# Performance work log

Hardware: AMD Instinct MI355X
Metric: run time of the kernel (lower is better)

## Reference

```python
import jax, jax.numpy as jnp
import numpy as np

INPUT_SIZE = 256
HIDDEN = 256


def setup_inputs() -> dict:
    key = jax.random.key(0)
    ks = jax.random.split(key, 9)
    B, T = 32, 2048
    d_in = INPUT_SIZE + HIDDEN
    s = 1.0 / np.sqrt(d_in)  # nn.Linear default init scale
    def W(k):
        return jax.random.uniform(k, (d_in, HIDDEN), jnp.float32, -s, s)
    def b(k):
        return jax.random.uniform(k, (HIDDEN,), jnp.float32, -s, s)
    return {
        "x": jax.random.normal(ks[0], (B, T, INPUT_SIZE), jnp.float32),
        "W_f": W(ks[1]), "b_f": b(ks[2]),
        "W_i": W(ks[3]), "b_i": b(ks[4]),
        "W_o": W(ks[5]), "b_o": b(ks[6]),
        "W_c": W(ks[7]), "b_c": b(ks[8]),
    }


def reference(x, W_f, b_f, W_i, b_i, W_o, b_o, W_c, b_c):
    B, T, _ = x.shape
    H = W_f.shape[1]
    # Fuse the 4 gate GEMMs into one [d_in, 4H] matmul (same math).
    W4 = jnp.concatenate([W_f, W_i, W_o, W_c], axis=1)  # [in+H, 4H]
    b4 = jnp.concatenate([b_f, b_i, b_o, b_c], axis=0)  # [4H]

    def step(carry, x_t):
        c, h = carry
        z = jnp.concatenate([x_t, h], axis=1) @ W4 + b4  # [B, 4H]
        f = jax.nn.sigmoid(z[:, 0 * H:1 * H])
        i = jax.nn.sigmoid(z[:, 1 * H:2 * H])
        o = jax.nn.sigmoid(z[:, 2 * H:3 * H])
        g = jnp.tanh(z[:, 3 * H:4 * H])
        c = f * c + i * g
        h = o * jnp.tanh(c)
        return (c, h), h

    c0 = jnp.zeros((B, H), x.dtype)
    h0 = jnp.zeros((B, H), x.dtype)
    _, hs = jax.lax.scan(step, (c0, h0), jnp.swapaxes(x, 0, 1))  # [T, B, H]
    # Original prepends each new hidden state, so output is in REVERSE time order.
    out = jnp.swapaxes(hs, 0, 1)[:, ::-1, :]  # [B, T, H]
    return out
```

## Files before the change

kernel.cpp:

```cpp
#include <hip/hip_runtime.h>
#include <cstdint>
#include <cstddef>

#define NB    32
#define NTT   2048
#define NIN   256
#define NH    256
#define NG    16
#define BLOCK 512
#define NHC   16

typedef __attribute__((ext_vector_type(8))) short    s8v;
typedef __attribute__((ext_vector_type(4))) float    f4v;
typedef __attribute__((ext_vector_type(4))) unsigned u4v;

__device__ __forceinline__ float u2f(unsigned u) {
    union { float f; unsigned u; } x; x.u = u; return x.f;
}
__device__ __forceinline__ unsigned cvt_pk_bf16(float s0, float s1) {
    unsigned r;
    asm("v_cvt_pk_bf16_f32 %0, %1, %2" : "=v"(r) : "v"(s0), "v"(s1));
    return r;
}
__device__ __forceinline__ void split2(float v0, float v1, unsigned& hp, unsigned& lp) {
    hp = cvt_pk_bf16(v0, v1);
    float h0 = u2f(hp << 16);
    float h1 = u2f(hp & 0xFFFF0000u);
    lp = cvt_pk_bf16(v0 - h0, v1 - h1);
}
__device__ __forceinline__ void split8(f4v a, f4v b, u4v& hw, u4v& lw) {
    unsigned h0,h1,h2,h3,l0,l1,l2,l3;
    split2(a[0], a[1], h0, l0);
    split2(a[2], a[3], h1, l1);
    split2(b[0], b[1], h2, l2);
    split2(b[2], b[3], h3, l3);
    hw = (u4v){h0,h1,h2,h3};
    lw = (u4v){l0,l1,l2,l3};
}
__device__ __forceinline__ float fast_sig(float v) {
    const float L2E = 1.4426950408889634f;
    return __builtin_amdgcn_rcpf(1.f + __builtin_amdgcn_exp2f(-L2E * v));
}
__device__ __forceinline__ float fast_tanh(float v) {
    const float L2E2 = 2.8853900817779268f;
    float e = __builtin_amdgcn_exp2f(L2E2 * v);
    return 1.f - 2.f * __builtin_amdgcn_rcpf(e + 1.f);
}

__device__ __forceinline__ u4v ld4_dev(const unsigned* p) {
    u4v v;
    asm volatile("global_load_dwordx4 %0, %1, off sc1" : "=v"(v) : "v"(p));
    return v;
}
__device__ __forceinline__ int ldf_dev(const int* p) {
    int v;
    asm volatile("global_load_dword %0, %1, off sc1\n\ts_waitcnt vmcnt(0)"
                 : "=v"(v) : "v"(p) : "memory");
    return v;
}
__device__ __forceinline__ void st_dev(unsigned* p, unsigned v) {
    asm volatile("global_store_dword %0, %1, off sc1" :: "v"(p), "v"(v) : "memory");
}
template<int OFF>
__device__ __forceinline__ void pf_ld4x2(const float* base, f4v& a, f4v& b) {
    asm volatile(
        "global_load_dwordx4 %0, %2, off offset:%c3\n\t"
        "global_load_dwordx4 %1, %2, off offset:%c4"
        : "=&v"(a), "=&v"(b)
        : "v"(base), "n"(OFF), "n"(OFF+16)
        : "memory");
}


__global__ __launch_bounds__(BLOCK, 1) void lstm_kernel(
    const float* __restrict__ x,
    const float* __restrict__ Wf, const float* __restrict__ bfp,
    const float* __restrict__ Wi, const float* __restrict__ bip,
    const float* __restrict__ Wo, const float* __restrict__ bop,
    const float* __restrict__ Wc, const float* __restrict__ bcp,
    float* __restrict__ out,
    unsigned* __restrict__ wsbase)
{
    __shared__ unsigned short Ahi[NB * 512];
    __shared__ unsigned short Alo[NB * 512];
    __shared__ float zbuf[32][68];

    char* AhiB = (char*)Ahi;
    char* AloB = (char*)Alo;
    const int wg   = blockIdx.x;
    const int tid  = threadIdx.x;
    const int lane = tid & 63;
    const int wv   = tid >> 6;
    const int mt   = wv & 1;
    const int nt   = wv >> 1;

    int* flags     = (int*)wsbase;
    unsigned* hbuf = wsbase + 1024;

    s8v bhi[16], blo[16];
    for (int p = 0; p < 2; ++p) {
        {
            const int lc   = tid >> 4;
            const int gate = 2 * p + (lc >> 4);
            const int col  = wg * NHC + (lc & 15);
            const float* W = (gate == 0) ? Wf : (gate == 1) ? Wi : (gate == 2) ? Wo : Wc;
            #pragma unroll
            for (int cj = 0; cj < 4; ++cj) {
                const int kc = (tid & 15) * 4 + cj;
                const int k0 = kc * 8;
                f4v a, b;
                #pragma unroll
                for (int e = 0; e < 4; ++e) a[e] = W[(size_t)(k0 + e) * NH + col];
                #pragma unroll
                for (int e = 0; e < 4; ++e) b[e] = W[(size_t)(k0 + 4 + e) * NH + col];
                u4v hwv, lwv;
                split8(a, b, hwv, lwv);
                *(u4v*)(AhiB + lc * 1024 + ((kc ^ (lc & 7)) << 4)) = hwv;
                *(u4v*)(AloB + lc * 1024 + ((kc ^ (lc & 7)) << 4)) = lwv;
            }
        }
        __syncthreads();
        if ((nt >> 1) == p) {
            const int brow = (nt & 1) * 16 + (lane & 15);
            const int bsub = lane >> 4;
            #pragma unroll
            for (int kt = 0; kt < 16; ++kt) {
                const int kc = kt * 4 + bsub;
                bhi[kt] = *(s8v*)(AhiB + brow * 1024 + ((kc ^ (brow & 7)) << 4));
                blo[kt] = *(s8v*)(AloB + brow * 1024 + ((kc ^ (brow & 7)) << 4));
            }
        }
        __syncthreads();
    }

    const int ub   = tid >> 4;
    const int ulh  = tid & 15;
    const int ucol = wg * NHC + ulh;
    const float bias_f = bfp[ucol];
    const float bias_i = bip[ucol];
    const float bias_o = bop[ucol];
    const float bias_c = bcp[ucol];
    float cst = 0.f;

    const int sb   = tid >> 4;
    const int sseg = tid & 15;

    const int arow = mt * 16 + (lane & 15);
    const int asub = lane >> 4;

    f4v xv[4];
    {
        const float* xr = x + (size_t)sb * NTT * NIN + sseg * 16;
        xv[0] = *(const f4v*)(xr);
        xv[1] = *(const f4v*)(xr + 4);
        xv[2] = *(const f4v*)(xr + 8);
        xv[3] = *(const f4v*)(xr + 12);
    }

    for (int t = 0; t < NTT; ++t) {
        #pragma unroll
        for (int j = 0; j < 2; ++j) {
            u4v hwv, lwv;
            split8(xv[2 * j], xv[2 * j + 1], hwv, lwv);
            const int kc = sseg * 2 + j;
            *(u4v*)(AhiB + sb * 1024 + ((kc ^ (sb & 7)) << 4)) = hwv;
            *(u4v*)(AloB + sb * 1024 + ((kc ^ (sb & 7)) << 4)) = lwv;
        }
        {
            const int tp = (t < NTT - 1) ? t + 1 : t;
            const float* xr = x + ((size_t)sb * NTT + tp) * NIN + sseg * 16;
            pf_ld4x2<0>(xr, xv[0], xv[1]);
            pf_ld4x2<32>(xr, xv[2], xv[3]);
        }
        __syncthreads();

        if (t > 0 && wv == 0 && lane < NG) {
            const int* fp = flags + lane;
            int it = 0;
            for (;;) {
                int v = ldf_dev(fp);
                if (!__any(v < t)) break;
                if (++it > 4096) break;
            }
        }
        __syncthreads();

        f4v acc0 = (f4v){0.f, 0.f, 0.f, 0.f};
        f4v acc1 = acc0, acc2 = acc0;

        if (t > 0) {
            const unsigned* hp = hbuf + (size_t)(t & 1) * (NB * NH)
                               + (size_t)sb * NH + sseg * 16;
            u4v w0 = ld4_dev(hp);
            u4v w1 = ld4_dev(hp + 4);
            u4v w2 = ld4_dev(hp + 8);
            u4v w3 = ld4_dev(hp + 12);

            #pragma unroll
            for (int kt = 0; kt < 8; ++kt) {
                const int kc = kt * 4 + asub;
                s8v ah = *(s8v*)(AhiB + arow * 1024 + ((kc ^ (arow & 7)) << 4));
                s8v al = *(s8v*)(AloB + arow * 1024 + ((kc ^ (arow & 7)) << 4));
                acc0 = __builtin_amdgcn_mfma_f32_16x16x32_bf16(ah, bhi[kt], acc0, 0, 0, 0);
                acc1 = __builtin_amdgcn_mfma_f32_16x16x32_bf16(ah, blo[kt], acc1, 0, 0, 0);
                acc2 = __builtin_amdgcn_mfma_f32_16x16x32_bf16(al, bhi[kt], acc2, 0, 0, 0);
            }

            asm volatile("s_waitcnt vmcnt(0)"
                         : "+v"(w0), "+v"(w1), "+v"(w2), "+v"(w3) :: "memory");
            u4v wA[2][2] = {{w0, w1}, {w2, w3}};
            #pragma unroll
            for (int j = 0; j < 2; ++j) {
                u4v hwv, lwv;
                hwv[0] = __builtin_amdgcn_perm(wA[j][0][1], wA[j][0][0], 0x05040100u);
                hwv[1] = __builtin_amdgcn_perm(wA[j][0][3], wA[j][0][2], 0x05040100u);
                hwv[2] = __builtin_amdgcn_perm(wA[j][1][1], wA[j][1][0], 0x05040100u);
                hwv[3] = __builtin_amdgcn_perm(wA[j][1][3], wA[j][1][2], 0x05040100u);
                lwv[0] = __builtin_amdgcn_perm(wA[j][0][1], wA[j][0][0], 0x07060302u);
                lwv[1] = __builtin_amdgcn_perm(wA[j][0][3], wA[j][0][2], 0x07060302u);
                lwv[2] = __builtin_amdgcn_perm(wA[j][1][1], wA[j][1][0], 0x07060302u);
                lwv[3] = __builtin_amdgcn_perm(wA[j][1][3], wA[j][1][2], 0x07060302u);
                const int kc = 32 + sseg * 2 + j;
                *(u4v*)(AhiB + sb * 1024 + ((kc ^ (sb & 7)) << 4)) = hwv;
                *(u4v*)(AloB + sb * 1024 + ((kc ^ (sb & 7)) << 4)) = lwv;
            }
        } else {
            #pragma unroll
            for (int kt = 0; kt < 8; ++kt) {
                const int kc = kt * 4 + asub;
                s8v ah = *(s8v*)(AhiB + arow * 1024 + ((kc ^ (arow & 7)) << 4));
                s8v al = *(s8v*)(AloB + arow * 1024 + ((kc ^ (arow & 7)) << 4));
                acc0 = __builtin_amdgcn_mfma_f32_16x16x32_bf16(ah, bhi[kt], acc0, 0, 0, 0);
                acc1 = __builtin_amdgcn_mfma_f32_16x16x32_bf16(ah, blo[kt], acc1, 0, 0, 0);
                acc2 = __builtin_amdgcn_mfma_f32_16x16x32_bf16(al, bhi[kt], acc2, 0, 0, 0);
            }
            const u4v zz = (u4v){0u, 0u, 0u, 0u};
            #pragma unroll
            for (int j = 0; j < 2; ++j) {
                const int kc = 32 + sseg * 2 + j;
                *(u4v*)(AhiB + sb * 1024 + ((kc ^ (sb & 7)) << 4)) = zz;
                *(u4v*)(AloB + sb * 1024 + ((kc ^ (sb & 7)) << 4)) = zz;
            }
        }
        __syncthreads();

        #pragma unroll
        for (int kt = 8; kt < 16; ++kt) {
            const int kc = kt * 4 + asub;
            s8v ah = *(s8v*)(AhiB + arow * 1024 + ((kc ^ (arow & 7)) << 4));
            s8v al = *(s8v*)(AloB + arow * 1024 + ((kc ^ (arow & 7)) << 4));
            acc0 = __builtin_amdgcn_mfma_f32_16x16x32_bf16(ah, bhi[kt], acc0, 0, 0, 0);
            acc1 = __builtin_amdgcn_mfma_f32_16x16x32_bf16(ah, blo[kt], acc1, 0, 0, 0);
            acc2 = __builtin_amdgcn_mfma_f32_16x16x32_bf16(al, bhi[kt], acc2, 0, 0, 0);
        }
        const f4v zv = acc0 + acc1 + acc2;

        {
            const int zc = nt * 16 + (lane & 15);
            const int rb = mt * 16 + (lane >> 4) * 4;
            #pragma unroll
            for (int j = 0; j < 4; ++j)
                zbuf[rb + j][zc] = zv[j];
        }
        __syncthreads();

        {
            const float zf = zbuf[ub][ulh]      + bias_f;
            const float zi = zbuf[ub][16 + ulh] + bias_i;
            const float zo = zbuf[ub][32 + ulh] + bias_o;
            const float zg = zbuf[ub][48 + ulh] + bias_c;
            const float fg = fast_sig(zf);
            const float ig = fast_sig(zi);
            const float og = fast_sig(zo);
            const float gg = fast_tanh(zg);
            cst = fg * cst + ig * gg;
            const float hv = og * fast_tanh(cst);
            out[((size_t)ub * NTT + (NTT - 1 - t)) * NH + ucol] = hv;
            unsigned p0  = cvt_pk_bf16(hv, 0.f);
            float   hif  = u2f(p0 << 16);
            unsigned w   = cvt_pk_bf16(hv, hv - hif);
            st_dev(hbuf + (size_t)((t + 1) & 1) * (NB * NH) + (size_t)ub * NH + ucol, w);
        }
        asm volatile("s_waitcnt vmcnt(0)"
                     : "+v"(xv[0]), "+v"(xv[1]), "+v"(xv[2]), "+v"(xv[3]) :: "memory");
        __syncthreads();
        if (tid == 0)
            st_dev((unsigned*)(flags + wg), (unsigned)(t + 1));
    }
}

extern "C" void kernel_launch(void* const* d_in, const int* in_sizes, int n_in,
                              void* d_out, int out_size, void* d_ws, size_t ws_size,
                              hipStream_t stream) {
    (void)in_sizes; (void)n_in; (void)out_size; (void)ws_size;
    const float* x  = (const float*)d_in[0];
    const float* Wf = (const float*)d_in[1];
    const float* bf = (const float*)d_in[2];
    const float* Wi = (const float*)d_in[3];
    const float* bi = (const float*)d_in[4];
    const float* Wo = (const float*)d_in[5];
    const float* bo = (const float*)d_in[6];
    const float* Wc = (const float*)d_in[7];
    const float* bc = (const float*)d_in[8];
    float* out = (float*)d_out;
    unsigned* ws = (unsigned*)d_ws;

    hipMemsetAsync(d_ws, 0, 4096, stream);

    lstm_kernel<<<NG, BLOCK, 0, stream>>>(x, Wf, bf, Wi, bi, Wo, bo, Wc, bc,
                                          out, ws);
}
```

Before: 7.763 ms.

## Replace flag barrier with timestep-tagged hidden-state atoms polled directly

Each hidden-state value is now stored as a 64-bit pair holding the bf16 hi/lo payload and the timestep tag. Consumers prefetch the next step's atoms right after computing, then spin only until every tag matches the expected step. This removes the separate per-workgroup flag store, the flag polling loop, one __syncthreads per step and the workspace memset. The input-part MFMAs now run before the wait. The cost is twice the bytes per hidden value and correctness that depends on tag validity without zeroing the workspace.

```diff
diff --git a/kernel.cpp b/kernel.cpp
--- a/kernel.cpp
+++ b/kernel.cpp
@@ -13,6 +13,7 @@
 typedef __attribute__((ext_vector_type(8))) short    s8v;
 typedef __attribute__((ext_vector_type(4))) float    f4v;
 typedef __attribute__((ext_vector_type(4))) unsigned u4v;
+typedef __attribute__((ext_vector_type(2))) unsigned u2v;
 
 __device__ __forceinline__ float u2f(unsigned u) {
     union { float f; unsigned u; } x; x.u = u; return x.f;
@@ -47,19 +48,27 @@
     return 1.f - 2.f * __builtin_amdgcn_rcpf(e + 1.f);
 }
 
-__device__ __forceinline__ u4v ld4_dev(const unsigned* p) {
-    u4v v;
-    asm volatile("global_load_dwordx4 %0, %1, off sc1" : "=v"(v) : "v"(p));
-    return v;
-}
-__device__ __forceinline__ int ldf_dev(const int* p) {
-    int v;
-    asm volatile("global_load_dword %0, %1, off sc1\n\ts_waitcnt vmcnt(0)"
-                 : "=v"(v) : "v"(p) : "memory");
-    return v;
-}
-__device__ __forceinline__ void st_dev(unsigned* p, unsigned v) {
-    asm volatile("global_store_dword %0, %1, off sc1" :: "v"(p), "v"(v) : "memory");
+template<int OFF>
+__device__ __forceinline__ void ld_atoms8(const unsigned long long* base,
+        u2v& a0, u2v& a1, u2v& a2, u2v& a3, u2v& a4, u2v& a5, u2v& a6, u2v& a7) {
+    asm volatile(
+        "global_load_dwordx2 %0, %8, off offset:%c9  sc1\n\t"
+        "global_load_dwordx2 %1, %8, off offset:%c10 sc1\n\t"
+        "global_load_dwordx2 %2, %8, off offset:%c11 sc1\n\t"
+        "global_load_dwordx2 %3, %8, off offset:%c12 sc1\n\t"
+        "global_load_dwordx2 %4, %8, off offset:%c13 sc1\n\t"
+        "global_load_dwordx2 %5, %8, off offset:%c14 sc1\n\t"
+        "global_load_dwordx2 %6, %8, off offset:%c15 sc1\n\t"
+        "global_load_dwordx2 %7, %8, off offset:%c16 sc1"
+        : "+v"(a0), "+v"(a1), "+v"(a2), "+v"(a3),
+          "+v"(a4), "+v"(a5), "+v"(a6), "+v"(a7)
+        : "v"(base), "n"(OFF), "n"(OFF+8), "n"(OFF+16), "n"(OFF+24),
+          "n"(OFF+32), "n"(OFF+40), "n"(OFF+48), "n"(OFF+56)
+        : "memory");
+}
+__device__ __forceinline__ void st_atom(unsigned long long* p, unsigned payload, unsigned tag) {
+    u2v v; v[0] = payload; v[1] = tag;
+    asm volatile("global_store_dwordx2 %0, %1, off sc1" :: "v"(p), "v"(v) : "memory");
 }
 template<int OFF>
 __device__ __forceinline__ void pf_ld4x2(const float* base, f4v& a, f4v& b) {
@@ -79,7 +88,7 @@
     const float* __restrict__ Wo, const float* __restrict__ bop,
     const float* __restrict__ Wc, const float* __restrict__ bcp,
     float* __restrict__ out,
-    unsigned* __restrict__ wsbase)
+    unsigned long long* __restrict__ hatoms)
 {
     __shared__ unsigned short Ahi[NB * 512];
     __shared__ unsigned short Alo[NB * 512];
@@ -93,9 +102,6 @@
     const int wv   = tid >> 6;
     const int mt   = wv & 1;
     const int nt   = wv >> 1;
-
-    int* flags     = (int*)wsbase;
-    unsigned* hbuf = wsbase + 1024;
 
     s8v bhi[16], blo[16];
     for (int p = 0; p < 2; ++p) {
@@ -148,6 +154,10 @@
     const int arow = mt * 16 + (lane & 15);
     const int asub = lane >> 4;
 
+    u2v hr[16];
+    #pragma unroll
+    for (int e = 0; e < 16; ++e) { hr[e][0] = 0u; hr[e][1] = 0u; }
+
     f4v xv[4];
     {
         const float* xr = x + (size_t)sb * NTT * NIN + sseg * 16;
@@ -156,6 +166,7 @@
         xv[2] = *(const f4v*)(xr + 8);
         xv[3] = *(const f4v*)(xr + 12);
     }
+    asm volatile("" : "+v"(xv[0]), "+v"(xv[1]), "+v"(xv[2]), "+v"(xv[3]));
 
     for (int t = 0; t < NTT; ++t) {
         #pragma unroll
@@ -174,66 +185,55 @@
         }
         __syncthreads();
 
-        if (t > 0 && wv == 0 && lane < NG) {
-            const int* fp = flags + lane;
-            int it = 0;
-            for (;;) {
-                int v = ldf_dev(fp);
-                if (!__any(v < t)) break;
-                if (++it > 4096) break;
-            }
-        }
-        __syncthreads();
-
         f4v acc0 = (f4v){0.f, 0.f, 0.f, 0.f};
         f4v acc1 = acc0, acc2 = acc0;
-
+        #pragma unroll
+        for (int kt = 0; kt < 8; ++kt) {
+            const int kc = kt * 4 + asub;
+            s8v ah = *(s8v*)(AhiB + arow * 1024 + ((kc ^ (arow & 7)) << 4));
+            s8v al = *(s8v*)(AloB + arow * 1024 + ((kc ^ (arow & 7)) << 4));
+            acc0 = __builtin_amdgcn_mfma_f32_16x16x32_bf16(ah, bhi[kt], acc0, 0, 0, 0);
+            acc1 = __builtin_amdgcn_mfma_f32_16x16x32_bf16(ah, blo[kt], acc1, 0, 0, 0);
+            acc2 = __builtin_amdgcn_mfma_f32_16x16x32_bf16(al, bhi[kt], acc2, 0, 0, 0);
+        }
+
+        asm volatile("s_waitcnt vmcnt(0)" ::: "memory");
+        __builtin_amdgcn_sched_barrier(0);
         if (t > 0) {
-            const unsigned* hp = hbuf + (size_t)(t & 1) * (NB * NH)
-                               + (size_t)sb * NH + sseg * 16;
-            u4v w0 = ld4_dev(hp);
-            u4v w1 = ld4_dev(hp + 4);
-            u4v w2 = ld4_dev(hp + 8);
-            u4v w3 = ld4_dev(hp + 12);
-
-            #pragma unroll
-            for (int kt = 0; kt < 8; ++kt) {
-                const int kc = kt * 4 + asub;
-                s8v ah = *(s8v*)(AhiB + arow * 1024 + ((kc ^ (arow & 7)) << 4));
-                s8v al = *(s8v*)(AloB + arow * 1024 + ((kc ^ (arow & 7)) << 4));
-                acc0 = __builtin_amdgcn_mfma_f32_16x16x32_bf16(ah, bhi[kt], acc0, 0, 0, 0);
-                acc1 = __builtin_amdgcn_mfma_f32_16x16x32_bf16(ah, blo[kt], acc1, 0, 0, 0);
-                acc2 = __builtin_amdgcn_mfma_f32_16x16x32_bf16(al, bhi[kt], acc2, 0, 0, 0);
-            }
-
-            asm volatile("s_waitcnt vmcnt(0)"
-                         : "+v"(w0), "+v"(w1), "+v"(w2), "+v"(w3) :: "memory");
-            u4v wA[2][2] = {{w0, w1}, {w2, w3}};
+            const unsigned texp = (unsigned)t;
+            unsigned d = 0;
+            #pragma unroll
+            for (int e = 0; e < 16; ++e) d |= (hr[e][1] ^ texp);
+            int guard = 0;
+            while (__any(d != 0)) {
+                if (++guard > 8192) break;
+                const unsigned long long* hp =
+                    hatoms + (size_t)(t & 1) * (NB * NH) + (size_t)sb * NH + sseg * 16;
+                ld_atoms8<0>(hp, hr[0], hr[1], hr[2], hr[3], hr[4], hr[5], hr[6], hr[7]);
+                ld_atoms8<64>(hp, hr[8], hr[9], hr[10], hr[11], hr[12], hr[13], hr[14], hr[15]);
+                asm volatile("s_waitcnt vmcnt(0)" ::: "memory");
+                __builtin_amdgcn_sched_barrier(0);
+                d = 0;
+                #pragma unroll
+                for (int e = 0; e < 16; ++e) d |= (hr[e][1] ^ texp);
+            }
             #pragma unroll
             for (int j = 0; j < 2; ++j) {
+                const int b0 = j * 8;
                 u4v hwv, lwv;
-                hwv[0] = __builtin_amdgcn_perm(wA[j][0][1], wA[j][0][0], 0x05040100u);
-                hwv[1] = __builtin_amdgcn_perm(wA[j][0][3], wA[j][0][2], 0x05040100u);
-                hwv[2] = __builtin_amdgcn_perm(wA[j][1][1], wA[j][1][0], 0x05040100u);
-                hwv[3] = __builtin_amdgcn_perm(wA[j][1][3], wA[j][1][2], 0x05040100u);
-                lwv[0] = __builtin_amdgcn_perm(wA[j][0][1], wA[j][0][0], 0x07060302u);
-                lwv[1] = __builtin_amdgcn_perm(wA[j][0][3], wA[j][0][2], 0x07060302u);
-                lwv[2] = __builtin_amdgcn_perm(wA[j][1][1], wA[j][1][0], 0x07060302u);
-                lwv[3] = __builtin_amdgcn_perm(wA[j][1][3], wA[j][1][2], 0x07060302u);
+                hwv[0] = __builtin_amdgcn_perm(hr[b0+1][0], hr[b0+0][0], 0x05040100u);
+                hwv[1] = __builtin_amdgcn_perm(hr[b0+3][0], hr[b0+2][0], 0x05040100u);
+                hwv[2] = __builtin_amdgcn_perm(hr[b0+5][0], hr[b0+4][0], 0x05040100u);
+                hwv[3] = __builtin_amdgcn_perm(hr[b0+7][0], hr[b0+6][0], 0x05040100u);
+                lwv[0] = __builtin_amdgcn_perm(hr[b0+1][0], hr[b0+0][0], 0x07060302u);
+                lwv[1] = __builtin_amdgcn_perm(hr[b0+3][0], hr[b0+2][0], 0x07060302u);
+                lwv[2] = __builtin_amdgcn_perm(hr[b0+5][0], hr[b0+4][0], 0x07060302u);
+                lwv[3] = __builtin_amdgcn_perm(hr[b0+7][0], hr[b0+6][0], 0x07060302u);
                 const int kc = 32 + sseg * 2 + j;
                 *(u4v*)(AhiB + sb * 1024 + ((kc ^ (sb & 7)) << 4)) = hwv;
                 *(u4v*)(AloB + sb * 1024 + ((kc ^ (sb & 7)) << 4)) = lwv;
             }
         } else {
-            #pragma unroll
-            for (int kt = 0; kt < 8; ++kt) {
-                const int kc = kt * 4 + asub;
-                s8v ah = *(s8v*)(AhiB + arow * 1024 + ((kc ^ (arow & 7)) << 4));
-                s8v al = *(s8v*)(AloB + arow * 1024 + ((kc ^ (arow & 7)) << 4));
-                acc0 = __builtin_amdgcn_mfma_f32_16x16x32_bf16(ah, bhi[kt], acc0, 0, 0, 0);
-                acc1 = __builtin_amdgcn_mfma_f32_16x16x32_bf16(ah, blo[kt], acc1, 0, 0, 0);
-                acc2 = __builtin_amdgcn_mfma_f32_16x16x32_bf16(al, bhi[kt], acc2, 0, 0, 0);
-            }
             const u4v zz = (u4v){0u, 0u, 0u, 0u};
             #pragma unroll
             for (int j = 0; j < 2; ++j) {
@@ -275,17 +275,19 @@
             const float gg = fast_tanh(zg);
             cst = fg * cst + ig * gg;
             const float hv = og * fast_tanh(cst);
-            out[((size_t)ub * NTT + (NTT - 1 - t)) * NH + ucol] = hv;
             unsigned p0  = cvt_pk_bf16(hv, 0.f);
             float   hif  = u2f(p0 << 16);
             unsigned w   = cvt_pk_bf16(hv, hv - hif);
-            st_dev(hbuf + (size_t)((t + 1) & 1) * (NB * NH) + (size_t)ub * NH + ucol, w);
-        }
-        asm volatile("s_waitcnt vmcnt(0)"
-                     : "+v"(xv[0]), "+v"(xv[1]), "+v"(xv[2]), "+v"(xv[3]) :: "memory");
-        __syncthreads();
-        if (tid == 0)
-            st_dev((unsigned*)(flags + wg), (unsigned)(t + 1));
+            st_atom(hatoms + (size_t)((t + 1) & 1) * (NB * NH) + (size_t)ub * NH + ucol,
+                    w, (unsigned)(t + 1));
+            out[((size_t)ub * NTT + (NTT - 1 - t)) * NH + ucol] = hv;
+        }
+        if (t < NTT - 1) {
+            const unsigned long long* hp =
+                hatoms + (size_t)((t + 1) & 1) * (NB * NH) + (size_t)sb * NH + sseg * 16;
+            ld_atoms8<0>(hp, hr[0], hr[1], hr[2], hr[3], hr[4], hr[5], hr[6], hr[7]);
+            ld_atoms8<64>(hp, hr[8], hr[9], hr[10], hr[11], hr[12], hr[13], hr[14], hr[15]);
+        }
     }
 }
 
@@ -303,10 +305,9 @@
     const float* Wc = (const float*)d_in[7];
     const float* bc = (const float*)d_in[8];
     float* out = (float*)d_out;
-    unsigned* ws = (unsigned*)d_ws;
-
-    hipMemsetAsync(d_ws, 0, 4096, stream);
+
+    unsigned long long* hatoms = (unsigned long long*)d_ws;
 
     lstm_kernel<<<NG, BLOCK, 0, stream>>>(x, Wf, bf, Wi, bi, Wo, bo, Wc, bc,
-                                          out, ws);
-}
+                                          out, hatoms);
+}
```

New measurement: 27.04 ms. 248% more time.
